# Performance work log

Measured on AMD Instinct MI355X. Metric: run time of the kernel, lower is better.

## Reference

```python
import jax, jax.numpy as jnp
import numpy as np

LN_EPS = 1e-5

def _layernorm(x, g, b):
    mu = jnp.mean(x, axis=-1, keepdims=True)
    var = jnp.mean(jnp.square(x - mu), axis=-1, keepdims=True)
    return (x - mu) * jax.lax.rsqrt(var + LN_EPS) * g + b

def setup_inputs() -> dict:
    key = jax.random.key(0)
    ks = jax.random.split(key, 8)
    b, n, h = 2, 64, 32
    edge_in = 1            # edge_dim(0) + 1
    mid = 128
    nc_in, nc_out, num_freq = 32, 32, 5   # degrees 2,2 -> to_order=5
    out_dim = nc_out * nc_in * num_freq   # 5120, rearranged '(o i f)'
    d_in = d_out = 5
    s1 = 1.0 / np.sqrt(edge_in)
    s2 = 1.0 / np.sqrt(mid)
    return {
        "feat": jax.random.normal(ks[0], (b, n, h, edge_in), jnp.float32),
        "basis": jax.random.normal(ks[1], (b, n, h, 1, d_out, 1, d_in, num_freq), jnp.float32),
        "W1": jax.random.normal(ks[2], (edge_in, mid), jnp.float32) * s1,
        "b1": jnp.zeros((mid,), jnp.float32),
        "g1": jnp.ones((mid,), jnp.float32),
        "beta1": jnp.zeros((mid,), jnp.float32),
        "W2": jax.random.normal(ks[3], (mid, mid), jnp.float32) * s2,
        "b2": jnp.zeros((mid,), jnp.float32),
        "g2": jnp.ones((mid,), jnp.float32),
        "beta2": jnp.zeros((mid,), jnp.float32),
        "W3": jax.random.normal(ks[4], (mid, out_dim), jnp.float32) * s2,
        "b3": jnp.zeros((out_dim,), jnp.float32),
    }

def reference(feat, basis, W1, b1, g1, beta1, W2, b2, g2, beta2, W3, b3):
    nc_out, nc_in, num_freq = 32, 32, 5
    # RadialFunc MLP: Linear -> LN -> ReLU -> Linear -> LN -> ReLU -> Linear
    x = jax.nn.relu(_layernorm(feat @ W1 + b1, g1, beta1))
    x = jax.nn.relu(_layernorm(x @ W2 + b2, g2, beta2))
    y = x @ W3 + b3                                   # (b,n,h, o*i*f)
    bb, nn_, hh = y.shape[0], y.shape[1], y.shape[2]
    R = y.reshape(bb, nn_, hh, nc_out, nc_in, num_freq)  # '(o i f)' split order
    B = basis[:, :, :, 0, :, 0, :, :]                 # (b,n,h,d_out,d_in,f)
    # fused broadcast-multiply-reduce over frequency axis f
    out = jnp.einsum('bnhoif,bnhdmf->bnhodim', R, B)  # (b,n,h,o,d_out,i,d_in)
    d_out, d_in = B.shape[3], B.shape[4]
    return out.reshape(bb, nn_, hh, nc_out * d_out, nc_in * d_in)
```

## Files before the change

### kernel.cpp

```cpp
#include <hip/hip_runtime.h>

#define LN_EPS 1e-5f

__global__ __launch_bounds__(256) void k1_mlp(
    const float* __restrict__ feat,
    const float* __restrict__ W1, const float* __restrict__ b1,
    const float* __restrict__ g1, const float* __restrict__ be1,
    const float* __restrict__ W2, const float* __restrict__ b2,
    const float* __restrict__ g2, const float* __restrict__ be2,
    float* __restrict__ x2out)
{
    const int ty = threadIdx.x >> 7;
    const int j  = threadIdx.x & 127;
    const int row = blockIdx.x * 2 + ty;

    __shared__ float sx1[2][128];
    __shared__ float sred[2][2][2];

    const float f = feat[row];
    float v = fmaf(f, W1[j], b1[j]);

    float s = v, q = v * v;
    #pragma unroll
    for (int off = 32; off > 0; off >>= 1) {
        s += __shfl_down(s, off);
        q += __shfl_down(q, off);
    }
    const int wir = j >> 6;
    if ((j & 63) == 0) { sred[ty][wir][0] = s; sred[ty][wir][1] = q; }
    __syncthreads();
    float sum = sred[ty][0][0] + sred[ty][1][0];
    float sq  = sred[ty][0][1] + sred[ty][1][1];
    float mu  = sum * (1.0f / 128.0f);
    float var = fmaf(-mu, mu, sq * (1.0f / 128.0f));
    float x1  = fmaf((v - mu) * rsqrtf(var + LN_EPS), g1[j], be1[j]);
    x1 = fmaxf(x1, 0.0f);
    sx1[ty][j] = x1;
    __syncthreads();

    float a = b2[j];
    #pragma unroll 8
    for (int k = 0; k < 128; ++k)
        a = fmaf(sx1[ty][k], W2[k * 128 + j], a);

    s = a; q = a * a;
    #pragma unroll
    for (int off = 32; off > 0; off >>= 1) {
        s += __shfl_down(s, off);
        q += __shfl_down(q, off);
    }
    if ((j & 63) == 0) { sred[ty][wir][0] = s; sred[ty][wir][1] = q; }
    __syncthreads();
    sum = sred[ty][0][0] + sred[ty][1][0];
    sq  = sred[ty][0][1] + sred[ty][1][1];
    mu  = sum * (1.0f / 128.0f);
    var = fmaf(-mu, mu, sq * (1.0f / 128.0f));
    float x2v = fmaf((a - mu) * rsqrtf(var + LN_EPS), g2[j], be2[j]);
    x2v = fmaxf(x2v, 0.0f);
    x2out[row * 128 + j] = x2v;
}

__global__ __launch_bounds__(256) void k2_gemm_einsum(
    const float* __restrict__ x2,
    const float* __restrict__ W3, const float* __restrict__ b3,
    const float* __restrict__ basis,
    float* __restrict__ out)
{
    const int tid = threadIdx.x;
    const int tx  = tid & 31;
    const int ty  = tid >> 5;
    const int row0 = blockIdx.x * 32;
    const int p0   = blockIdx.y * 128;

    __shared__ float sX[128][36];
    __shared__ float sB[32 * 125];

    {
        const int r  = tid >> 3;
        const int k0 = (tid & 7) * 16;
        const float4* src = (const float4*)(x2 + (size_t)(row0 + r) * 128 + k0);
        #pragma unroll
        for (int jj = 0; jj < 4; ++jj) {
            float4 vv = src[jj];
            sX[k0 + jj * 4 + 0][r] = vv.x;
            sX[k0 + jj * 4 + 1][r] = vv.y;
            sX[k0 + jj * 4 + 2][r] = vv.z;
            sX[k0 + jj * 4 + 3][r] = vv.w;
        }
    }
    for (int idx = tid; idx < 32 * 125; idx += 256)
        sB[idx] = basis[(size_t)row0 * 125 + idx];
    __syncthreads();

    float acc[4][20];
    {
        const float4* bp = (const float4*)(b3 + p0 * 5 + tx * 20);
        float4 q0 = bp[0], q1 = bp[1], q2 = bp[2], q3 = bp[3], q4 = bp[4];
        const float bb[20] = {q0.x, q0.y, q0.z, q0.w, q1.x, q1.y, q1.z, q1.w,
                              q2.x, q2.y, q2.z, q2.w, q3.x, q3.y, q3.z, q3.w,
                              q4.x, q4.y, q4.z, q4.w};
        #pragma unroll
        for (int r = 0; r < 4; ++r)
            #pragma unroll
            for (int c = 0; c < 20; ++c)
                acc[r][c] = bb[c];
    }

    const float* w3p = W3 + p0 * 5 + tx * 20;
    #pragma unroll 2
    for (int k = 0; k < 128; ++k) {
        const float4* wr = (const float4*)(w3p + (size_t)k * 5120);
        float4 w0 = wr[0], w1 = wr[1], w2 = wr[2], w3v = wr[3], w4 = wr[4];
        const float wc[20] = {w0.x, w0.y, w0.z, w0.w, w1.x, w1.y, w1.z, w1.w,
                              w2.x, w2.y, w2.z, w2.w, w3v.x, w3v.y, w3v.z, w3v.w,
                              w4.x, w4.y, w4.z, w4.w};
        const float4 xv = *(const float4*)&sX[k][ty * 4];
        const float xs[4] = {xv.x, xv.y, xv.z, xv.w};
        #pragma unroll
        for (int r = 0; r < 4; ++r)
            #pragma unroll
            for (int c = 0; c < 20; ++c)
                acc[r][c] = fmaf(xs[r], wc[c], acc[r][c]);
    }

    const int pb = p0 + tx * 4;
    const int o  = pb >> 5;
    const int i0 = pb & 31;

    #pragma unroll
    for (int rs = 0; rs < 4; ++rs) {
        const int rl = ty * 4 + rs;
        float* orow = out + (size_t)(row0 + rl) * 25600 + (size_t)o * 800 + i0 * 5;
        const float* Br = sB + rl * 125;
        #pragma unroll
        for (int d = 0; d < 5; ++d) {
            float Bv[25];
            #pragma unroll
            for (int qq = 0; qq < 25; ++qq) Bv[qq] = Br[d * 25 + qq];
            float vv[20];
            #pragma unroll
            for (int p = 0; p < 4; ++p) {
                #pragma unroll
                for (int m = 0; m < 5; ++m) {
                    float t = acc[rs][p * 5 + 0] * Bv[m * 5 + 0];
                    t = fmaf(acc[rs][p * 5 + 1], Bv[m * 5 + 1], t);
                    t = fmaf(acc[rs][p * 5 + 2], Bv[m * 5 + 2], t);
                    t = fmaf(acc[rs][p * 5 + 3], Bv[m * 5 + 3], t);
                    t = fmaf(acc[rs][p * 5 + 4], Bv[m * 5 + 4], t);
                    vv[p * 5 + m] = t;
                }
            }
            float4* dst = (float4*)(orow + d * 160);
            dst[0] = make_float4(vv[0],  vv[1],  vv[2],  vv[3]);
            dst[1] = make_float4(vv[4],  vv[5],  vv[6],  vv[7]);
            dst[2] = make_float4(vv[8],  vv[9],  vv[10], vv[11]);
            dst[3] = make_float4(vv[12], vv[13], vv[14], vv[15]);
            dst[4] = make_float4(vv[16], vv[17], vv[18], vv[19]);
        }
    }
}

extern "C" void kernel_launch(void* const* d_in, const int* in_sizes, int n_in,
                              void* d_out, int out_size, void* d_ws, size_t ws_size,
                              hipStream_t stream)
{
    const float* feat  = (const float*)d_in[0];
    const float* basis = (const float*)d_in[1];
    const float* W1    = (const float*)d_in[2];
    const float* b1    = (const float*)d_in[3];
    const float* g1    = (const float*)d_in[4];
    const float* be1   = (const float*)d_in[5];
    const float* W2    = (const float*)d_in[6];
    const float* b2    = (const float*)d_in[7];
    const float* g2    = (const float*)d_in[8];
    const float* be2   = (const float*)d_in[9];
    const float* W3    = (const float*)d_in[10];
    const float* b3    = (const float*)d_in[11];

    float* out = (float*)d_out;
    float* x2  = (float*)d_ws;

    const int rows = 4096;

    k1_mlp<<<rows / 2, 256, 0, stream>>>(feat, W1, b1, g1, be1, W2, b2, g2, be2, x2);

    dim3 grid(rows / 32, 8);
    k2_gemm_einsum<<<grid, 256, 0, stream>>>(x2, W3, b3, basis, out);
}
```

Before: 607.1 us.

## Split W3 GEMM into bf16 MFMA kernel with repacked operands, separate einsum

Replaces the FP32 FMA-based third linear layer with a bf16 MFMA 32x32x16 GEMM. Activations and W3 are first repacked into MFMA-fragment layouts, then the einsum runs in its own kernel that reads the GEMM result from a workspace buffer. This targets the compute cost of the fp32 GEMM. In exchange it adds a 4096x5120 fp32 intermediate round trip through global memory, extra launches, and bf16 rounding error in the inputs.

```diff
diff --git a/kernel.cpp b/kernel.cpp
--- a/kernel.cpp
+++ b/kernel.cpp
@@ -1,6 +1,15 @@
 #include <hip/hip_runtime.h>
 
 #define LN_EPS 1e-5f
+
+typedef __attribute__((ext_vector_type(8)))  short bf16x8;
+typedef __attribute__((ext_vector_type(16))) float floatx16;
+
+static __device__ __forceinline__ unsigned short f2bf(float x) {
+    union { float f; unsigned u; } v; v.f = x;
+    unsigned r = v.u + 0x7FFFu + ((v.u >> 16) & 1u);
+    return (unsigned short)(r >> 16);
+}
 
 __global__ __launch_bounds__(256) void k1_mlp(
     const float* __restrict__ feat,
@@ -60,10 +69,90 @@
     x2out[row * 128 + j] = x2v;
 }
 
-__global__ __launch_bounds__(256) void k2_gemm_einsum(
-    const float* __restrict__ x2,
-    const float* __restrict__ W3, const float* __restrict__ b3,
-    const float* __restrict__ basis,
+__global__ __launch_bounds__(256) void k_repack_x(
+    const float* __restrict__ x2, unsigned int* __restrict__ A)
+{
+    const int g = blockIdx.x * 256 + threadIdx.x;
+    const int L = g & 63;
+    const int s = (g >> 6) & 7;
+    const int R = g >> 9;
+    const int row = R * 32 + (L & 31);
+    const int kb  = s * 16 + (L >> 5) * 8;
+    const float4* src = (const float4*)(x2 + (size_t)row * 128 + kb);
+    float4 a = src[0], b = src[1];
+    uint4 w;
+    w.x = f2bf(a.x) | ((unsigned)f2bf(a.y) << 16);
+    w.y = f2bf(a.z) | ((unsigned)f2bf(a.w) << 16);
+    w.z = f2bf(b.x) | ((unsigned)f2bf(b.y) << 16);
+    w.w = f2bf(b.z) | ((unsigned)f2bf(b.w) << 16);
+    ((uint4*)A)[g] = w;
+}
+
+__global__ __launch_bounds__(256) void k_repack_w(
+    const float* __restrict__ W3, unsigned int* __restrict__ B)
+{
+    const int g = blockIdx.x * 256 + threadIdx.x;
+    const int L = g & 63;
+    const int s = (g >> 6) & 7;
+    const int t = g >> 9;
+    const int n  = t * 32 + (L & 31);
+    const int kb = s * 16 + (L >> 5) * 8;
+    unsigned short o[8];
+    #pragma unroll
+    for (int j = 0; j < 8; ++j)
+        o[j] = f2bf(W3[(size_t)(kb + j) * 5120 + n]);
+    uint4 w;
+    w.x = o[0] | ((unsigned)o[1] << 16);
+    w.y = o[2] | ((unsigned)o[3] << 16);
+    w.z = o[4] | ((unsigned)o[5] << 16);
+    w.w = o[6] | ((unsigned)o[7] << 16);
+    ((uint4*)B)[g] = w;
+}
+
+__global__ __launch_bounds__(256) void k_gemm(
+    const unsigned int* __restrict__ Abf, const unsigned int* __restrict__ Bbf,
+    const float* __restrict__ b3, float* __restrict__ Y)
+{
+    const int lane = threadIdx.x & 63;
+    const int w    = threadIdx.x >> 6;
+    const int R    = blockIdx.x;
+    const int cb   = blockIdx.y;
+    const int t0   = cb * 20 + w * 5;
+
+    floatx16 acc[5];
+    #pragma unroll
+    for (int tt = 0; tt < 5; ++tt) acc[tt] = (floatx16)0.0f;
+
+    const uint4* Ap = (const uint4*)Abf + (size_t)R * 512 + lane;
+    const uint4* Bp = (const uint4*)Bbf + (size_t)t0 * 512 + lane;
+
+    #pragma unroll
+    for (int s = 0; s < 8; ++s) {
+        bf16x8 a = *(const bf16x8*)(Ap + s * 64);
+        #pragma unroll
+        for (int tt = 0; tt < 5; ++tt) {
+            bf16x8 b = *(const bf16x8*)(Bp + (size_t)tt * 512 + s * 64);
+            acc[tt] = __builtin_amdgcn_mfma_f32_32x32x16_bf16(a, b, acc[tt], 0, 0, 0);
+        }
+    }
+
+    const int m_hi = 4 * (lane >> 5);
+    const int nl   = lane & 31;
+    float* yb = Y + (size_t)R * 32 * 5120;
+    #pragma unroll
+    for (int tt = 0; tt < 5; ++tt) {
+        const int n = (t0 + tt) * 32 + nl;
+        const float bias = b3[n];
+        #pragma unroll
+        for (int reg = 0; reg < 16; ++reg) {
+            const int m = (reg & 3) + 8 * (reg >> 2) + m_hi;
+            yb[(size_t)m * 5120 + n] = acc[tt][reg] + bias;
+        }
+    }
+}
+
+__global__ __launch_bounds__(256) void k_einsum(
+    const float* __restrict__ Y, const float* __restrict__ basis,
     float* __restrict__ out)
 {
     const int tid = threadIdx.x;
@@ -72,55 +161,22 @@
     const int row0 = blockIdx.x * 32;
     const int p0   = blockIdx.y * 128;
 
-    __shared__ float sX[128][36];
     __shared__ float sB[32 * 125];
-
-    {
-        const int r  = tid >> 3;
-        const int k0 = (tid & 7) * 16;
-        const float4* src = (const float4*)(x2 + (size_t)(row0 + r) * 128 + k0);
-        #pragma unroll
-        for (int jj = 0; jj < 4; ++jj) {
-            float4 vv = src[jj];
-            sX[k0 + jj * 4 + 0][r] = vv.x;
-            sX[k0 + jj * 4 + 1][r] = vv.y;
-            sX[k0 + jj * 4 + 2][r] = vv.z;
-            sX[k0 + jj * 4 + 3][r] = vv.w;
-        }
-    }
     for (int idx = tid; idx < 32 * 125; idx += 256)
         sB[idx] = basis[(size_t)row0 * 125 + idx];
     __syncthreads();
 
     float acc[4][20];
-    {
-        const float4* bp = (const float4*)(b3 + p0 * 5 + tx * 20);
-        float4 q0 = bp[0], q1 = bp[1], q2 = bp[2], q3 = bp[3], q4 = bp[4];
-        const float bb[20] = {q0.x, q0.y, q0.z, q0.w, q1.x, q1.y, q1.z, q1.w,
-                              q2.x, q2.y, q2.z, q2.w, q3.x, q3.y, q3.z, q3.w,
-                              q4.x, q4.y, q4.z, q4.w};
-        #pragma unroll
-        for (int r = 0; r < 4; ++r)
-            #pragma unroll
-            for (int c = 0; c < 20; ++c)
-                acc[r][c] = bb[c];
-    }
-
-    const float* w3p = W3 + p0 * 5 + tx * 20;
-    #pragma unroll 2
-    for (int k = 0; k < 128; ++k) {
-        const float4* wr = (const float4*)(w3p + (size_t)k * 5120);
-        float4 w0 = wr[0], w1 = wr[1], w2 = wr[2], w3v = wr[3], w4 = wr[4];
-        const float wc[20] = {w0.x, w0.y, w0.z, w0.w, w1.x, w1.y, w1.z, w1.w,
-                              w2.x, w2.y, w2.z, w2.w, w3v.x, w3v.y, w3v.z, w3v.w,
-                              w4.x, w4.y, w4.z, w4.w};
-        const float4 xv = *(const float4*)&sX[k][ty * 4];
-        const float xs[4] = {xv.x, xv.y, xv.z, xv.w};
-        #pragma unroll
-        for (int r = 0; r < 4; ++r)
-            #pragma unroll
-            for (int c = 0; c < 20; ++c)
-                acc[r][c] = fmaf(xs[r], wc[c], acc[r][c]);
+    #pragma unroll
+    for (int r = 0; r < 4; ++r) {
+        const float4* yp = (const float4*)(Y + (size_t)(row0 + ty * 4 + r) * 5120
+                                             + p0 * 5 + tx * 20);
+        float4 q0 = yp[0], q1 = yp[1], q2 = yp[2], q3 = yp[3], q4 = yp[4];
+        acc[r][0]=q0.x;  acc[r][1]=q0.y;  acc[r][2]=q0.z;  acc[r][3]=q0.w;
+        acc[r][4]=q1.x;  acc[r][5]=q1.y;  acc[r][6]=q1.z;  acc[r][7]=q1.w;
+        acc[r][8]=q2.x;  acc[r][9]=q2.y;  acc[r][10]=q2.z; acc[r][11]=q2.w;
+        acc[r][12]=q3.x; acc[r][13]=q3.y; acc[r][14]=q3.z; acc[r][15]=q3.w;
+        acc[r][16]=q4.x; acc[r][17]=q4.y; acc[r][18]=q4.z; acc[r][19]=q4.w;
     }
 
     const int pb = p0 + tx * 4;
@@ -178,12 +234,22 @@
     const float* b3    = (const float*)d_in[11];
 
     float* out = (float*)d_out;
-    float* x2  = (float*)d_ws;
+
+    char* ws = (char*)d_ws;
+    float*        x2  = (float*)(ws);
+    unsigned int* Abf = (unsigned int*)(ws + 2097152);
+    unsigned int* Bbf = (unsigned int*)(ws + 3145728);
+    float*        Yt  = (float*)(ws + 4456448);
 
     const int rows = 4096;
 
     k1_mlp<<<rows / 2, 256, 0, stream>>>(feat, W1, b1, g1, be1, W2, b2, g2, be2, x2);
-
-    dim3 grid(rows / 32, 8);
-    k2_gemm_einsum<<<grid, 256, 0, stream>>>(x2, W3, b3, basis, out);
-}
+    k_repack_x<<<256, 256, 0, stream>>>(x2, Abf);
+    k_repack_w<<<320, 256, 0, stream>>>(W3, Bbf);
+
+    dim3 ggrid(rows / 32, 8);
+    k_gemm<<<ggrid, 256, 0, stream>>>(Abf, Bbf, b3, Yt);
+
+    dim3 egrid(rows / 32, 8);
+    k_einsum<<<egrid, 256, 0, stream>>>(Yt, basis, out);
+}
```

Measured after the change: 560.7 us. 1.08x faster.
